# Performance work log

Hardware: AMD Instinct MI355X
Metric: run time of the kernel (lower is better)

Reference implementation:

```python
import jax, jax.numpy as jnp
import numpy as np

E = 1024   # embed_dim
H = 16     # num_heads
D = E // H # head_dim
B = 2
S = 2048
YAT_EPS = 0.1


def setup_inputs() -> dict:
    key = jax.random.key(0)
    ks = jax.random.split(key, 5)
    w_scale = (6.0 / (E + E)) ** 0.5  # xavier_uniform bound
    def xavier(k):
        return jax.random.uniform(k, (E, E), jnp.float32, -w_scale, w_scale)
    return {
        "x": jax.random.normal(ks[0], (B, S, E), jnp.float32),
        "Wq": xavier(ks[1]), "bq": jnp.zeros((E,), jnp.float32),
        "Wk": xavier(ks[2]), "bk": jnp.zeros((E,), jnp.float32),
        "Wv": xavier(ks[3]), "bv": jnp.zeros((E,), jnp.float32),
        "Wo": xavier(ks[4]), "bo": jnp.zeros((E,), jnp.float32),
    }


def reference(x, Wq, bq, Wk, bk, Wv, bv, Wo, bo):
    b, s, _ = x.shape
    # Projections (Linear: x @ W + b, flax kernel layout [in, out])
    Q = x @ Wq + bq
    K = x @ Wk + bk
    V = x @ Wv + bv
    # [B, H, S, D]
    Q = Q.reshape(b, s, H, D).transpose(0, 2, 1, 3)
    K = K.reshape(b, s, H, D).transpose(0, 2, 1, 3)
    V = V.reshape(b, s, H, D).transpose(0, 2, 1, 3)
    # L2 normalize along head_dim
    Qn = Q / (jnp.linalg.norm(Q, axis=-1, keepdims=True) + 1e-8)
    Kn = K / (jnp.linalg.norm(K, axis=-1, keepdims=True) + 1e-8)
    # Yat kernel scores: (1 + <q,k>)^2 / (eps + (1 - <q,k>))
    dot = jnp.einsum("bhqd,bhkd->bhqk", Qn, Kn)
    scores = (1.0 + dot) ** 2 / (YAT_EPS + (1.0 - dot))
    # Sum-normalize (no softmax)
    attn = scores / (jnp.sum(scores, axis=-1, keepdims=True) + 1e-6)
    out = jnp.einsum("bhqk,bhkd->bhqd", attn, V)
    out = out.transpose(0, 2, 1, 3).reshape(b, s, E)
    return out @ Wo + bo
```

## Files before the change

kernel.cpp:

```cpp
#include <hip/hip_runtime.h>
#include <math.h>

#define EDIM 1024
#define NH   16
#define HD   64
#define BATCH 2
#define SEQ  2048
#define NROW (BATCH*SEQ)
#define YAT_EPS 0.1f

typedef _Float16 f16;
typedef _Float16 f16x8 __attribute__((ext_vector_type(8)));
typedef _Float16 f16x4 __attribute__((ext_vector_type(4)));
typedef __fp16   h16x2 __attribute__((ext_vector_type(2)));
typedef float    f32x4 __attribute__((ext_vector_type(4)));

static __device__ __forceinline__ int pk2(float a, float b) {
    union { h16x2 h; int i; } u;
    u.h = __builtin_amdgcn_cvt_pkrtz(a, b);
    return u.i;
}

__global__ __launch_bounds__(256)
void prep_kernel(const float* __restrict__ x, f16* __restrict__ xb,
                 const float* __restrict__ W0, const float* __restrict__ W1,
                 const float* __restrict__ W2, const float* __restrict__ W3,
                 f16* __restrict__ T0, f16* __restrict__ T1,
                 f16* __restrict__ T2, f16* __restrict__ T3)
{
    const int z = blockIdx.z;
    if (z == 4) {
        const int bid = blockIdx.y * 32 + blockIdx.x;
#pragma unroll
        for (int i = 0; i < 4; ++i) {
            const int off = bid * 4096 + i * 1024 + threadIdx.x * 4;
            const float4 v = *(const float4*)(x + off);
            union { int i2[2]; f16x4 h; } o;
            o.i2[0] = pk2(v.x, v.y);
            o.i2[1] = pk2(v.z, v.w);
            *(f16x4*)(xb + off) = o.h;
        }
        return;
    }
    const float* W = (z == 0) ? W0 : (z == 1) ? W1 : (z == 2) ? W2 : W3;
    f16*         Wt = (z == 0) ? T0 : (z == 1) ? T1 : (z == 2) ? T2 : T3;

    __shared__ float T[32][33];
    const int t = threadIdx.x;
    const int r = t >> 3, c4 = (t & 7) * 4;
    const int bi = blockIdx.x * 32, bj = blockIdx.y * 32;
    const float4 v = *(const float4*)(W + (size_t)(bi + r) * 1024 + bj + c4);
    T[r][c4 + 0] = v.x; T[r][c4 + 1] = v.y; T[r][c4 + 2] = v.z; T[r][c4 + 3] = v.w;
    __syncthreads();
    f16x4 o = {(f16)T[c4 + 0][r], (f16)T[c4 + 1][r], (f16)T[c4 + 2][r], (f16)T[c4 + 3][r]};
    *(f16x4*)(Wt + (size_t)(bj + r) * 1024 + bi + c4) = o;
}

template<int BM, int BN, int WM>
__global__ __launch_bounds__(WM * 128, 3)
void gemm_f16(const f16* __restrict__ A,
              const f16* __restrict__ B0, const f16* __restrict__ B1, const f16* __restrict__ B2,
              const float* __restrict__ bi0, const float* __restrict__ bi1, const float* __restrict__ bi2,
              void* __restrict__ o0, void* __restrict__ o1, void* __restrict__ o2,
              int e0, int e1, int e2)
{
    constexpr int NT    = WM * 128;
    constexpr int SR    = NT / 4;
    constexpr int ASL   = BM / SR;
    constexpr int BSL   = BN / SR;
    constexpr int ABUF  = BM * 32;
    constexpr int BBUF  = BN * 32;
    constexpr int WROWS = BM / WM;
    constexpr int MT    = WROWS / 16;
    constexpr int HALVES = BN / 128;
    constexpr int SCH    = 2048 / NT;
    __shared__ __align__(16) char lds[2 * (ABUF + BBUF) * 2];
    f16* As = (f16*)lds;
    f16* Bs = (f16*)lds + 2 * ABUF;

    const int z = blockIdx.z;
    const f16*   Bt   = (z == 0) ? B0  : (z == 1) ? B1  : B2;
    const float* bias = (z == 0) ? bi0 : (z == 1) ? bi1 : bi2;
    void*        Cout = (z == 0) ? o0  : (z == 1) ? o1  : o2;
    const int    epi  = (z == 0) ? e0  : (z == 1) ? e1  : e2;

    const int tid  = threadIdx.x;
    const int lane = tid & 63;
    const int w    = tid >> 6;
    const int cl   = lane & 15;
    const int quad = lane >> 4;
    const int wm = w % WM, wn = w / WM;
    const int bm = blockIdx.x * BM, bn = blockIdx.y * BN;
    const int wmoff = wm * WROWS;

    const int srow = tid >> 2;
    const int sc   = tid & 3;
    const int ssw  = (sc ^ (srow & 3)) * 8;
    const f16* gA = A  + (size_t)(bm + srow) * 1024 + sc * 8;
    const f16* gB = Bt + (size_t)(bn + srow) * 1024 + sc * 8;
    int lAo[ASL], lBo[BSL];
#pragma unroll
    for (int i = 0; i < ASL; ++i) lAo[i] = (srow + i * SR) * 32 + ssw;
#pragma unroll
    for (int i = 0; i < BSL; ++i) lBo[i] = (srow + i * SR) * 32 + ssw;

    f32x4 acc[MT][4];
#pragma unroll
    for (int i = 0; i < MT; ++i)
#pragma unroll
        for (int j = 0; j < 4; ++j) acc[i][j] = (f32x4){0.f, 0.f, 0.f, 0.f};

    f16x8 ra[ASL], rb[BSL];

#pragma unroll
    for (int i = 0; i < ASL; ++i) ra[i] = *(const f16x8*)(gA + (size_t)i * SR * 1024);
#pragma unroll
    for (int i = 0; i < BSL; ++i) rb[i] = *(const f16x8*)(gB + (size_t)i * SR * 1024);
#pragma unroll
    for (int i = 0; i < ASL; ++i) *(f16x8*)(As + lAo[i]) = ra[i];
#pragma unroll
    for (int i = 0; i < BSL; ++i) *(f16x8*)(Bs + lBo[i]) = rb[i];
#pragma unroll
    for (int i = 0; i < ASL; ++i) ra[i] = *(const f16x8*)(gA + (size_t)i * SR * 1024 + 32);
#pragma unroll
    for (int i = 0; i < BSL; ++i) rb[i] = *(const f16x8*)(gB + (size_t)i * SR * 1024 + 32);
    __syncthreads();

    const int fsw = (quad ^ (cl & 3)) * 8;

    for (int it = 0; it < 32; ++it) {
        const int buf = it & 1, nb = buf ^ 1;
        if (it < 31) {
#pragma unroll
            for (int i = 0; i < ASL; ++i) *(f16x8*)(As + nb * ABUF + lAo[i]) = ra[i];
#pragma unroll
            for (int i = 0; i < BSL; ++i) *(f16x8*)(Bs + nb * BBUF + lBo[i]) = rb[i];
        }
        if (it < 30) {
            const int kn = (it + 2) * 32;
#pragma unroll
            for (int i = 0; i < ASL; ++i) ra[i] = *(const f16x8*)(gA + (size_t)i * SR * 1024 + kn);
#pragma unroll
            for (int i = 0; i < BSL; ++i) rb[i] = *(const f16x8*)(gB + (size_t)i * SR * 1024 + kn);
        }
        f16x8 af[MT], bf[4];
#pragma unroll
        for (int mt = 0; mt < MT; ++mt)
            af[mt] = *(const f16x8*)(&As[buf * ABUF + (wmoff + mt * 16 + cl) * 32 + fsw]);
#pragma unroll
        for (int nt = 0; nt < 4; ++nt)
            bf[nt] = *(const f16x8*)(&Bs[buf * BBUF + (wn * 64 + nt * 16 + cl) * 32 + fsw]);
#pragma unroll
        for (int mt = 0; mt < MT; ++mt)
#pragma unroll
            for (int nt = 0; nt < 4; ++nt)
                acc[mt][nt] = __builtin_amdgcn_mfma_f32_16x16x32_f16(af[mt], bf[nt], acc[mt][nt], 0, 0, 0);
        __syncthreads();
    }

    float bcol[4];
#pragma unroll
    for (int nt = 0; nt < 4; ++nt) bcol[nt] = bias[bn + wn * 64 + nt * 16 + cl];
#pragma unroll
    for (int mt = 0; mt < MT; ++mt)
#pragma unroll
        for (int nt = 0; nt < 4; ++nt)
#pragma unroll
            for (int rg = 0; rg < 4; ++rg) acc[mt][nt][rg] += bcol[nt];

    const int b_idx = bm >> 11, sl0 = bm & (SEQ - 1), h0 = bn >> 6;

    if (epi == 0) {
        float* C = (float*)Cout;
#pragma unroll
        for (int mt = 0; mt < MT; ++mt)
#pragma unroll
            for (int rg = 0; rg < 4; ++rg) {
                const int row = bm + wmoff + mt * 16 + quad * 4 + rg;
#pragma unroll
                for (int nt = 0; nt < 4; ++nt)
                    C[(size_t)row * EDIM + bn + wn * 64 + nt * 16 + cl] = acc[mt][nt][rg];
            }
    } else if (epi == 1) {
        if constexpr (BM == 128) {
        f16* C = (f16*)Cout;
        f16* S = (f16*)lds;
#pragma unroll
        for (int h = 0; h < HALVES; ++h) {
            __syncthreads();
            if ((wn >> 1) == h) {
#pragma unroll
                for (int mt = 0; mt < MT; ++mt)
#pragma unroll
                    for (int rg = 0; rg < 4; ++rg) {
                        float ss = 0.f;
#pragma unroll
                        for (int nt = 0; nt < 4; ++nt) ss += acc[mt][nt][rg] * acc[mt][nt][rg];
                        ss += __shfl_xor(ss, 1); ss += __shfl_xor(ss, 2);
                        ss += __shfl_xor(ss, 4); ss += __shfl_xor(ss, 8);
                        const float inv = 1.0f / (sqrtf(ss) + 1e-8f);
                        const int row = wmoff + mt * 16 + quad * 4 + rg;
#pragma unroll
                        for (int nt = 0; nt < 4; ++nt) {
                            const int colh = (wn & 1) * 64 + nt * 16 + cl;
                            S[row * 128 + (((colh >> 3) ^ (row & 15)) * 8) + (colh & 7)] =
                                (f16)(acc[mt][nt][rg] * inv);
                        }
                    }
            }
            __syncthreads();
#pragma unroll
            for (int i = 0; i < SCH; ++i) {
                const int c = tid + i * NT;
                const int s = c >> 4, gi = c & 15;
                f16x8 v = *(const f16x8*)(&S[s * 128 + ((gi ^ (s & 15)) * 8)]);
                const int head = h0 + h * 2 + (gi >> 3), d8 = (gi & 7) * 8;
                *(f16x8*)(C + ((size_t)(b_idx * NH + head) * SEQ + sl0 + s) * HD + d8) = v;
            }
        }
        }
    } else {
        if constexpr (BM == 128) {
        f16* C = (f16*)Cout;
        f16* S = (f16*)lds;
#pragma unroll
        for (int h = 0; h < HALVES; ++h) {
            __syncthreads();
            if ((wn >> 1) == h) {
#pragma unroll
                for (int mt = 0; mt < MT; ++mt) {
                    const int s0 = wmoff + mt * 16 + quad * 4;
#pragma unroll
                    for (int nt = 0; nt < 4; ++nt) {
                        const int colh = (wn & 1) * 64 + nt * 16 + cl;
                        f16x4 o = {(f16)acc[mt][nt][0], (f16)acc[mt][nt][1],
                                   (f16)acc[mt][nt][2], (f16)acc[mt][nt][3]};
                        *(f16x4*)(&S[colh * 128 + (((s0 >> 3) ^ (colh & 15)) * 8) + (s0 & 7)]) = o;
                    }
                }
            }
            __syncthreads();
#pragma unroll
            for (int i = 0; i < SCH; ++i) {
                const int c = tid + i * NT;
                const int colh = c >> 4, gi = c & 15;
                f16x8 v = *(const f16x8*)(&S[colh * 128 + ((gi ^ (colh & 15)) * 8)]);
                const int head = h0 + h * 2 + (colh >> 6), d = colh & 63;
                *(f16x8*)(C + ((size_t)(b_idx * NH + head) * HD + d) * SEQ + sl0 + gi * 8) = v;
            }
        }
        }
    }
}

__global__ __launch_bounds__(512, 4)
void yat_attn(const f16* __restrict__ Qh, const f16* __restrict__ Kh,
              const f16* __restrict__ Vt, f16* __restrict__ AO)
{
    __shared__ __align__(16) char lds[65536];
    f16* KB = (f16*)lds;
    f16* VB = (f16*)(lds + 32768);

    const int tid  = threadIdx.x;
    const int lane = tid & 63;
    const int w    = tid >> 6;
    const int cl   = lane & 15;
    const int quad = lane >> 4;
    const int wm = w & 3;
    const int wk = w >> 2;
    const int q0 = blockIdx.x * 128;
    const int bh = blockIdx.y;

    const f16* Qg = Qh + (size_t)bh * SEQ * HD;
    const f16* Kg = Kh + (size_t)bh * SEQ * HD;
    const f16* Vg = Vt + (size_t)bh * HD * SEQ;

    const int rk = tid >> 3;
    const int gk = tid & 7;
    const f16* gK = Kg + (size_t)rk * HD + gk * 8;
    const int kOff = rk * 64 + ((gk ^ (rk & 7)) * 8);
    const int rv = tid >> 4;
    const int gv = tid & 15;
    const f16* gV = Vg + (size_t)rv * SEQ + gv * 8;
    const int vOff = rv * 128 + ((gv ^ (rv & 15)) * 8);

    f16x8 kr0 = *(const f16x8*)(gK);
    f16x8 kr1 = *(const f16x8*)(gK + 64 * HD);
    f16x8 vr0 = *(const f16x8*)(gV);
    f16x8 vr1 = *(const f16x8*)(gV + (size_t)32 * SEQ);

    f16x8 qf[2][2];
#pragma unroll
    for (int qt = 0; qt < 2; ++qt)
#pragma unroll
        for (int kb = 0; kb < 2; ++kb)
            qf[qt][kb] = *(const f16x8*)(Qg + (size_t)(q0 + wm * 32 + qt * 16 + cl) * HD +
                                         (kb * 4 + quad) * 8);

    f32x4 O[2][4];
    float rs[2] = {0.f, 0.f};
#pragma unroll
    for (int i = 0; i < 2; ++i)
#pragma unroll
        for (int j = 0; j < 4; ++j) O[i][j] = (f32x4){0.f, 0.f, 0.f, 0.f};

    for (int t = 0; t < 16; ++t) {
        const int buf = t & 1;
        f16* Ks = KB + buf * 8192;
        f16* Vs = VB + buf * 8192;
        *(f16x8*)(Ks + kOff)        = kr0;
        *(f16x8*)(Ks + kOff + 4096) = kr1;
        *(f16x8*)(Vs + vOff)        = vr0;
        *(f16x8*)(Vs + vOff + 4096) = vr1;
        if (t < 15) {
            const f16* nK = gK + (size_t)(t + 1) * 128 * HD;
            const f16* nV = gV + (t + 1) * 128;
            kr0 = *(const f16x8*)(nK);
            kr1 = *(const f16x8*)(nK + 64 * HD);
            vr0 = *(const f16x8*)(nV);
            vr1 = *(const f16x8*)(nV + (size_t)32 * SEQ);
        }
        __syncthreads();

#pragma unroll
        for (int kt = 0; kt < 4; ++kt) {
            const int krow = (wk * 64 + kt * 16 + cl) * 64;
            f16x8 a0 = *(const f16x8*)(&Ks[krow + ((quad     ^ (cl & 7)) * 8)]);
            f16x8 a1 = *(const f16x8*)(&Ks[krow + (((4 + quad) ^ (cl & 7)) * 8)]);
            f32x4 s0 = (f32x4){0.f, 0.f, 0.f, 0.f};
            f32x4 s1 = (f32x4){0.f, 0.f, 0.f, 0.f};
            __builtin_amdgcn_s_setprio(1);
            s0 = __builtin_amdgcn_mfma_f32_16x16x32_f16(a0, qf[0][0], s0, 0, 0, 0);
            s0 = __builtin_amdgcn_mfma_f32_16x16x32_f16(a1, qf[0][1], s0, 0, 0, 0);
            s1 = __builtin_amdgcn_mfma_f32_16x16x32_f16(a0, qf[1][0], s1, 0, 0, 0);
            s1 = __builtin_amdgcn_mfma_f32_16x16x32_f16(a1, qf[1][1], s1, 0, 0, 0);
            __builtin_amdgcn_s_setprio(0);

            f16x4 pa0, pa1;
            {
                float p0[4], p1[4];
#pragma unroll
                for (int rg = 0; rg < 4; ++rg) {
                    const float u0 = (1.0f + YAT_EPS) - s0[rg];
                    const float u1 = (1.0f + YAT_EPS) - s1[rg];
                    p0[rg] = fmaf(4.41f, __builtin_amdgcn_rcpf(u0), u0 - 4.2f);
                    p1[rg] = fmaf(4.41f, __builtin_amdgcn_rcpf(u1), u1 - 4.2f);
                    rs[0] += p0[rg];
                    rs[1] += p1[rg];
                }
                union { int i2[2]; f16x4 h; } pk_;
                pk_.i2[0] = pk2(p0[0], p0[1]); pk_.i2[1] = pk2(p0[2], p0[3]);
                pa0 = pk_.h;
                pk_.i2[0] = pk2(p1[0], p1[1]); pk_.i2[1] = pk2(p1[2], p1[3]);
                pa1 = pk_.h;
            }

            const int g = wk * 8 + kt * 2 + (quad >> 1);
            __builtin_amdgcn_s_setprio(1);
#pragma unroll
            for (int dn = 0; dn < 4; ++dn) {
                const int row = dn * 16 + cl;
                f16x4 vb = *(const f16x4*)(&Vs[row * 128 + ((g ^ (row & 15)) * 8) + (quad & 1) * 4]);
                O[0][dn] = __builtin_amdgcn_mfma_f32_16x16x16f16(pa0, vb, O[0][dn], 0, 0, 0);
                O[1][dn] = __builtin_amdgcn_mfma_f32_16x16x16f16(pa1, vb, O[1][dn], 0, 0, 0);
            }
            __builtin_amdgcn_s_setprio(0);
        }
        __syncthreads();
    }

    float* rs_s = (float*)lds;
    float* Ox   = (float*)(lds + 1024);

#pragma unroll
    for (int qt = 0; qt < 2; ++qt) {
        float t = rs[qt];
        t += __shfl_xor(t, 16);
        t += __shfl_xor(t, 32);
        if (quad == 0) rs_s[wk * 128 + wm * 32 + qt * 16 + cl] = t;
    }
    if (wk == 1) {
#pragma unroll
        for (int qt = 0; qt < 2; ++qt)
#pragma unroll
            for (int dn = 0; dn < 4; ++dn)
#pragma unroll
                for (int rg = 0; rg < 4; ++rg)
                    Ox[(wm * 32 + qt * 16 + quad * 4 + rg) * 64 + dn * 16 + cl] = O[qt][dn][rg];
    }
    __syncthreads();
    if (wk == 0) {
        const int b = bh >> 4, h = bh & 15;
#pragma unroll
        for (int qt = 0; qt < 2; ++qt)
#pragma unroll
            for (int rg = 0; rg < 4; ++rg) {
                const int ql = wm * 32 + qt * 16 + quad * 4 + rg;
                const float tot = rs_s[ql] + rs_s[128 + ql];
                const float inv = 1.0f / (tot + 1e-6f);
                const size_t rowoff = ((size_t)b * SEQ + q0 + ql) * EDIM + h * 64;
#pragma unroll
                for (int dn = 0; dn < 4; ++dn)
                    AO[rowoff + dn * 16 + cl] =
                        (f16)((O[qt][dn][rg] + Ox[ql * 64 + dn * 16 + cl]) * inv);
            }
    }
}

extern "C" void kernel_launch(void* const* d_in, const int* in_sizes, int n_in,
                              void* d_out, int out_size, void* d_ws, size_t ws_size,
                              hipStream_t stream)
{
    const float* x  = (const float*)d_in[0];
    const float* Wq = (const float*)d_in[1];
    const float* bq = (const float*)d_in[2];
    const float* Wk = (const float*)d_in[3];
    const float* bk = (const float*)d_in[4];
    const float* Wv = (const float*)d_in[5];
    const float* bv = (const float*)d_in[6];
    const float* Wo = (const float*)d_in[7];
    const float* bo = (const float*)d_in[8];

    char* p = (char*)d_ws;
    f16* xb  = (f16*)p;                 p += (size_t)NROW * EDIM * 2;
    f16* Wqt = (f16*)p;                 p += (size_t)EDIM * EDIM * 2;
    f16* Wkt = (f16*)p;                 p += (size_t)EDIM * EDIM * 2;
    f16* Wvt = (f16*)p;                 p += (size_t)EDIM * EDIM * 2;
    f16* Wot = (f16*)p;                 p += (size_t)EDIM * EDIM * 2;
    f16* Qhb = (f16*)p;                 p += (size_t)NROW * EDIM * 2;
    f16* Khb = (f16*)p;                 p += (size_t)NROW * EDIM * 2;
    f16* Vtb = (f16*)p;                 p += (size_t)NROW * EDIM * 2;
    f16* AOb = (f16*)p;                 p += (size_t)NROW * EDIM * 2;

    prep_kernel<<<dim3(32, 32, 5), 256, 0, stream>>>(x, xb, Wq, Wk, Wv, Wo,
                                                     Wqt, Wkt, Wvt, Wot);

    gemm_f16<128, 128, 4><<<dim3(NROW / 128, EDIM / 128, 3), 512, 0, stream>>>(
        xb, Wqt, Wkt, Wvt, bq, bk, bv, Qhb, Khb, Vtb, 1, 1, 2);

    yat_attn<<<dim3(SEQ / 128, BATCH * NH), 512, 0, stream>>>(Qhb, Khb, Vtb, AOb);

    gemm_f16<64, 128, 2><<<dim3(NROW / 64, EDIM / 128, 1), 256, 0, stream>>>(
        AOb, Wot, Wot, Wot, bo, bo, bo, d_out, d_out, d_out, 0, 0, 0);
}
```

Measured before the change: 226.7 us.

## Stream GEMM tiles directly to LDS and relax attention occupancy bound

The projection GEMM now uses global_load_lds to copy A/B tiles straight from global memory into the double-buffered LDS. The XOR swizzle moves from the LDS store address to the global read address. This removes the register staging and separate LDS stores, at the cost of a shorter prefetch distance (one tile ahead instead of two). The attention kernel's launch bound drops from 4 to 2 waves-per-EU hints, giving the compiler more registers. A per-iteration barrier is moved out of its KV loop, which removes a sync but risks a race if that loop reuses LDS buffers.

```diff
diff --git a/kernel.cpp b/kernel.cpp
--- a/kernel.cpp
+++ b/kernel.cpp
@@ -19,6 +19,13 @@
     union { h16x2 h; int i; } u;
     u.h = __builtin_amdgcn_cvt_pkrtz(a, b);
     return u.i;
+}
+
+static __device__ __forceinline__ void gload16(const f16* g, f16* l) {
+    __builtin_amdgcn_global_load_lds(
+        (const __attribute__((address_space(1))) void*)g,
+        (__attribute__((address_space(3))) void*)l,
+        16, 0, 0);
 }
 
 __global__ __launch_bounds__(256)
@@ -95,14 +102,14 @@
 
     const int srow = tid >> 2;
     const int sc   = tid & 3;
-    const int ssw  = (sc ^ (srow & 3)) * 8;
-    const f16* gA = A  + (size_t)(bm + srow) * 1024 + sc * 8;
-    const f16* gB = Bt + (size_t)(bn + srow) * 1024 + sc * 8;
-    int lAo[ASL], lBo[BSL];
-#pragma unroll
-    for (int i = 0; i < ASL; ++i) lAo[i] = (srow + i * SR) * 32 + ssw;
-#pragma unroll
-    for (int i = 0; i < BSL; ++i) lBo[i] = (srow + i * SR) * 32 + ssw;
+    const int scg  = (sc ^ (srow & 3)) * 8;
+    const f16* gA = A  + (size_t)(bm + srow) * 1024 + scg;
+    const f16* gB = Bt + (size_t)(bn + srow) * 1024 + scg;
+    f16* lA[ASL]; f16* lB[BSL];
+#pragma unroll
+    for (int i = 0; i < ASL; ++i) lA[i] = As + (srow + i * SR) * 32 + sc * 8;
+#pragma unroll
+    for (int i = 0; i < BSL; ++i) lB[i] = Bs + (srow + i * SR) * 32 + sc * 8;
 
     f32x4 acc[MT][4];
 #pragma unroll
@@ -110,20 +117,10 @@
 #pragma unroll
         for (int j = 0; j < 4; ++j) acc[i][j] = (f32x4){0.f, 0.f, 0.f, 0.f};
 
-    f16x8 ra[ASL], rb[BSL];
-
-#pragma unroll
-    for (int i = 0; i < ASL; ++i) ra[i] = *(const f16x8*)(gA + (size_t)i * SR * 1024);
-#pragma unroll
-    for (int i = 0; i < BSL; ++i) rb[i] = *(const f16x8*)(gB + (size_t)i * SR * 1024);
-#pragma unroll
-    for (int i = 0; i < ASL; ++i) *(f16x8*)(As + lAo[i]) = ra[i];
-#pragma unroll
-    for (int i = 0; i < BSL; ++i) *(f16x8*)(Bs + lBo[i]) = rb[i];
-#pragma unroll
-    for (int i = 0; i < ASL; ++i) ra[i] = *(const f16x8*)(gA + (size_t)i * SR * 1024 + 32);
-#pragma unroll
-    for (int i = 0; i < BSL; ++i) rb[i] = *(const f16x8*)(gB + (size_t)i * SR * 1024 + 32);
+#pragma unroll
+    for (int i = 0; i < ASL; ++i) gload16(gA + (size_t)i * SR * 1024, lA[i]);
+#pragma unroll
+    for (int i = 0; i < BSL; ++i) gload16(gB + (size_t)i * SR * 1024, lB[i]);
     __syncthreads();
 
     const int fsw = (quad ^ (cl & 3)) * 8;
@@ -131,17 +128,13 @@
     for (int it = 0; it < 32; ++it) {
         const int buf = it & 1, nb = buf ^ 1;
         if (it < 31) {
-#pragma unroll
-            for (int i = 0; i < ASL; ++i) *(f16x8*)(As + nb * ABUF + lAo[i]) = ra[i];
-#pragma unroll
-            for (int i = 0; i < BSL; ++i) *(f16x8*)(Bs + nb * BBUF + lBo[i]) = rb[i];
-        }
-        if (it < 30) {
-            const int kn = (it + 2) * 32;
-#pragma unroll
-            for (int i = 0; i < ASL; ++i) ra[i] = *(const f16x8*)(gA + (size_t)i * SR * 1024 + kn);
-#pragma unroll
-            for (int i = 0; i < BSL; ++i) rb[i] = *(const f16x8*)(gB + (size_t)i * SR * 1024 + kn);
+            const int kn = (it + 1) * 32;
+#pragma unroll
+            for (int i = 0; i < ASL; ++i)
+                gload16(gA + (size_t)i * SR * 1024 + kn, lA[i] + nb * ABUF);
+#pragma unroll
+            for (int i = 0; i < BSL; ++i)
+                gload16(gB + (size_t)i * SR * 1024 + kn, lB[i] + nb * BBUF);
         }
         f16x8 af[MT], bf[4];
 #pragma unroll
@@ -253,7 +246,7 @@
     }
 }
 
-__global__ __launch_bounds__(512, 4)
+__global__ __launch_bounds__(512, 2)
 void yat_attn(const f16* __restrict__ Qh, const f16* __restrict__ Kh,
               const f16* __restrict__ Vt, f16* __restrict__ AO)
 {
@@ -366,9 +359,9 @@
             }
             __builtin_amdgcn_s_setprio(0);
         }
-        __syncthreads();
-    }
-
+    }
+
+    __syncthreads();
     float* rs_s = (float*)lds;
     float* Ox   = (float*)(lds + 1024);
 
```

Result: faster. 202.1 us (-10.9%).
